# Kernel tuning notes

Hardware: AMD Instinct MI355X
Metric: run time of the kernel (lower is better)

The kernel has to match this reference:

```python
import jax, jax.numpy as jnp
import numpy as np

B, NF, NB, E = 32768, 64, 33, 64  # batch, num_features, boundaries per feature, embedding size


def setup_inputs() -> dict:
    key = jax.random.key(0)
    kx, kb, kw = jax.random.split(key, 3)
    X = jax.random.normal(kx, (B, NF), dtype=jnp.float32)
    # strictly increasing per-feature boundaries: cumsum of positive steps
    steps = jax.random.uniform(kb, (NF, NB), dtype=jnp.float32, minval=0.05, maxval=0.2)
    bounds = jnp.cumsum(steps, axis=1) - 2.0  # roughly centered around the data range
    W = jax.random.normal(kw, (NF, NB - 1, E), dtype=jnp.float32) / np.sqrt(NB - 1).astype(np.float32)
    b = jnp.zeros((NF, E), dtype=jnp.float32)
    return {"X": X, "bounds": bounds, "W": W, "b": b}


def reference(X, bounds, W, b):
    # Piecewise-linear bin encoding, vectorized over all features at once.
    lo = bounds[:, :-1]            # [NF, NB-1]
    hi = bounds[:, 1:]             # [NF, NB-1]
    scale = hi - lo                # [NF, NB-1]
    x = X[:, :, None]              # [B, NF, 1]
    enc = (jax.nn.relu(x - lo[None]) - jax.nn.relu(x - hi[None])) / scale  # [B, NF, NB-1]
    # Per-feature Linear + ReLU (block-diagonal / grouped GEMM), then concat over features
    out = jax.nn.relu(jnp.einsum('bfi,fie->bfe', enc, W) + b[None])       # [B, NF, E]
    return out.reshape(X.shape[0], -1)                                     # [B, NF*E]
```

## Files before the change

### kernel.cpp

```cpp
#include <hip/hip_runtime.h>

#define B_TOT 32768
#define NF    64
#define NB    33
#define NSEG  32
#define E     64
#define BPB   256

__global__ __launch_bounds__(256) void pwl_kernel(
    const float* __restrict__ X,
    const float* __restrict__ bounds,
    const float* __restrict__ W,
    const float* __restrict__ bias,
    float* __restrict__ out)
{
    __shared__ __align__(16) float4 sPW[NSEG][E / 2];
    __shared__ float sBounds[NB];
    __shared__ uint2 sJF[BPB];

    const int f   = blockIdx.x;
    const int tid = threadIdx.x;
    const int b0  = blockIdx.y * BPB;

    const float x = X[(size_t)(b0 + tid) * NF + f];
    float biasv = 0.0f;
    if (tid < E) biasv = bias[f * E + tid];

    {
        const float2* Wg  = reinterpret_cast<const float2*>(W + f * (NSEG * E));
        float*        flat = &sPW[0][0].x;
        #pragma unroll
        for (int t = 0; t < 4; ++t) {
            const int idx = tid + t * 256;
            const float2 w2 = Wg[idx];
            *reinterpret_cast<float2*>(flat + idx * 4 + 2) = w2;
        }
        if (tid < NB) sBounds[tid] = bounds[f * NB + tid];
    }
    __syncthreads();

    {
        int c = 0;
        #pragma unroll
        for (int i = 0; i < NB; ++i) c += (sBounds[i] <= x) ? 1 : 0;
        int j = c - 1;
        j = (j < 0) ? 0 : ((j > NSEG - 1) ? NSEG - 1 : j);
        const float lo = sBounds[j];
        const float hi = sBounds[j + 1];
        float fr = (x - lo) / (hi - lo);
        fr = fminf(fmaxf(fr, 0.0f), 1.0f);
        sJF[tid] = make_uint2((unsigned)j, __float_as_uint(fr));
    }

    if (tid < E) {
        const int e2 = tid >> 1;
        const int c  = tid & 1;
        float acc = biasv;
        float* flat = &sPW[0][0].x;
        #pragma unroll
        for (int i = 0; i < NSEG; ++i) {
            float* cell = flat + (i * 32 + e2) * 4;
            const float w = cell[2 + c];
            cell[c] = acc;
            acc += w;
        }
    }
    __syncthreads();

    const int lane  = tid & 63;
    const int wv    = tid >> 6;
    const int half  = lane >> 5;
    const int e2    = lane & 31;
    const int wbase = wv * 64;

    const float4* __restrict__ PW = &sPW[0][0];
    float2* outp = reinterpret_cast<float2*>(
        out + (size_t)(b0 + wbase + half) * (NF * E) + f * E + 2 * e2);

    #pragma unroll 8
    for (int it = 0; it < 32; ++it) {
        const uint2 jf = sJF[wbase + 2 * it + half];
        const int   j  = (int)jf.x;
        const float fr = __uint_as_float(jf.y);
        const float4 v = PW[j * 32 + e2];
        float2 r;
        r.x = fmaxf(fmaf(fr, v.z, v.x), 0.0f);
        r.y = fmaxf(fmaf(fr, v.w, v.y), 0.0f);
        *outp = r;
        outp += 4096;
    }
}

extern "C" void kernel_launch(void* const* d_in, const int* in_sizes, int n_in,
                              void* d_out, int out_size, void* d_ws, size_t ws_size,
                              hipStream_t stream) {
    const float* X      = (const float*)d_in[0];
    const float* bounds = (const float*)d_in[1];
    const float* W      = (const float*)d_in[2];
    const float* bias   = (const float*)d_in[3];
    float* out          = (float*)d_out;

    dim3 grid(NF, B_TOT / BPB);
    dim3 block(256);
    pwl_kernel<<<grid, block, 0, stream>>>(X, bounds, W, bias, out);
}
```

Before: 539.4 us.

## Precompute prefix-sum table in workspace and write full contiguous output rows per block

A small pre-kernel builds the per-feature prefix-sum and slope table (bias-folded) once into workspace memory. The main kernel then assigns blocks to 16 batch rows across all features, so each row's 16 KB output is written contiguously with 16-byte nontemporal stores, and X is read as coalesced float4. This replaces the previous per-feature blocks, which wrote strided 256-byte pieces per row and rebuilt the table in shared memory in every block. In exchange, table lookups now go to global/L2 memory instead of LDS, and there is an extra launch. A fallback path keeps the old kernel when no workspace is available.

```diff
diff --git a/kernel.cpp b/kernel.cpp
--- a/kernel.cpp
+++ b/kernel.cpp
@@ -5,13 +5,112 @@
 #define NB    33
 #define NSEG  32
 #define E     64
-#define BPB   256
-
-__global__ __launch_bounds__(256) void pwl_kernel(
+#define RPB   16
+#define TBL_BYTES (NF * NSEG * (E / 2) * 16)
+
+typedef float v4f __attribute__((ext_vector_type(4)));
+
+__global__ __launch_bounds__(256) void build_table(
+    const float* __restrict__ W, const float* __restrict__ bias,
+    float4* __restrict__ tbl)
+{
+    __shared__ __align__(16) float sW[NSEG][E];
+    __shared__ __align__(16) float sP[NSEG][E];
+    const int f = blockIdx.x, tid = threadIdx.x;
+
+    const float4* Wg  = reinterpret_cast<const float4*>(W + f * (NSEG * E));
+    float4*       sW4 = reinterpret_cast<float4*>(&sW[0][0]);
+    sW4[tid]       = Wg[tid];
+    sW4[tid + 256] = Wg[tid + 256];
+    __syncthreads();
+
+    if (tid < E) {
+        float acc = bias[f * E + tid];
+        #pragma unroll
+        for (int j = 0; j < NSEG; ++j) { sP[j][tid] = acc; acc += sW[j][tid]; }
+    }
+    __syncthreads();
+
+    #pragma unroll
+    for (int t = 0; t < 4; ++t) {
+        const int rec = tid + t * 256;
+        const int j = rec >> 5, e2 = rec & 31;
+        tbl[f * 1024 + rec] =
+            make_float4(sP[j][2 * e2], sP[j][2 * e2 + 1],
+                        sW[j][2 * e2], sW[j][2 * e2 + 1]);
+    }
+}
+
+__global__ __launch_bounds__(256) void pwl_main(
     const float* __restrict__ X,
     const float* __restrict__ bounds,
-    const float* __restrict__ W,
-    const float* __restrict__ bias,
+    const float4* __restrict__ tbl,
+    float* __restrict__ out)
+{
+    __shared__ float sB[NF][NB];
+    __shared__ uint2 sJF[RPB][NF];
+
+    const int tid = threadIdx.x;
+    const int r0  = blockIdx.x * RPB;
+
+    for (int i = tid; i < NF * NB; i += 256) sB[0][i] = bounds[i];
+
+    const int rA = tid >> 4, q4 = tid & 15;
+    const float4 x4 =
+        reinterpret_cast<const float4*>(X)[(size_t)(r0 + rA) * (NF / 4) + q4];
+    __syncthreads();
+
+    {
+        const float xs[4] = {x4.x, x4.y, x4.z, x4.w};
+        #pragma unroll
+        for (int cc = 0; cc < 4; ++cc) {
+            const int   f = q4 * 4 + cc;
+            const float x = xs[cc];
+            int c = 0;
+            #pragma unroll
+            for (int i = 0; i < NB; ++i) c += (sB[f][i] <= x) ? 1 : 0;
+            int j = c - 1;
+            j = (j < 0) ? 0 : ((j > NSEG - 1) ? NSEG - 1 : j);
+            const float lo = sB[f][j];
+            const float hi = sB[f][j + 1];
+            float fr = (x - lo) / (hi - lo);
+            fr = fminf(fmaxf(fr, 0.0f), 1.0f);
+            sJF[rA][f] = make_uint2((unsigned)j, __float_as_uint(fr));
+        }
+    }
+    __syncthreads();
+
+    const int f = tid >> 2;
+    const int q = tid & 3;
+    const float4* tf = tbl + f * 1024 + q * 8;
+    v4f* out4 = reinterpret_cast<v4f*>(out) +
+                (size_t)r0 * (NF * E / 4) + f * 16 + q * 4;
+
+    #pragma unroll 2
+    for (int it = 0; it < RPB; ++it) {
+        const uint2 jf = sJF[it][f];
+        const float fr = __uint_as_float(jf.y);
+        const float4* __restrict__ rec = tf + jf.x * 32;
+        v4f o[4];
+        #pragma unroll
+        for (int m = 0; m < 4; ++m) {
+            const float4 a = rec[2 * m];
+            const float4 b = rec[2 * m + 1];
+            o[m][0] = fmaxf(fmaf(fr, a.z, a.x), 0.0f);
+            o[m][1] = fmaxf(fmaf(fr, a.w, a.y), 0.0f);
+            o[m][2] = fmaxf(fmaf(fr, b.z, b.x), 0.0f);
+            o[m][3] = fmaxf(fmaf(fr, b.w, b.y), 0.0f);
+        }
+        #pragma unroll
+        for (int m = 0; m < 4; ++m)
+            __builtin_nontemporal_store(o[m], out4 + (size_t)it * (NF * E / 4) + m);
+    }
+}
+
+#define BPB 256
+__global__ __launch_bounds__(256) void pwl_fallback(
+    const float* __restrict__ X, const float* __restrict__ bounds,
+    const float* __restrict__ W, const float* __restrict__ bias,
     float* __restrict__ out)
 {
     __shared__ __align__(16) float4 sPW[NSEG][E / 2];
@@ -27,7 +126,7 @@
     if (tid < E) biasv = bias[f * E + tid];
 
     {
-        const float2* Wg  = reinterpret_cast<const float2*>(W + f * (NSEG * E));
+        const float2* Wg   = reinterpret_cast<const float2*>(W + f * (NSEG * E));
         float*        flat = &sPW[0][0].x;
         #pragma unroll
         for (int t = 0; t < 4; ++t) {
@@ -100,7 +199,12 @@
     const float* bias   = (const float*)d_in[3];
     float* out          = (float*)d_out;
 
-    dim3 grid(NF, B_TOT / BPB);
-    dim3 block(256);
-    pwl_kernel<<<grid, block, 0, stream>>>(X, bounds, W, bias, out);
-}
+    if (ws_size >= (size_t)TBL_BYTES && d_ws != nullptr) {
+        float4* tbl = (float4*)d_ws;
+        build_table<<<dim3(NF), dim3(256), 0, stream>>>(W, bias, tbl);
+        pwl_main<<<dim3(B_TOT / RPB), dim3(256), 0, stream>>>(X, bounds, tbl, out);
+    } else {
+        dim3 grid(NF, B_TOT / BPB);
+        pwl_fallback<<<grid, dim3(256), 0, stream>>>(X, bounds, W, bias, out);
+    }
+}
```

After: 1.132 ms. 110% more time.
